# Performance work log

Hardware: AMD Instinct MI355X
Metric: run time of the kernel (lower is better)

## Reference

```python
import jax, jax.numpy as jnp
from jax import lax
import numpy as np

B, L, T = 128, 4096, 48


def setup_inputs() -> dict:
    key = jax.random.key(0)
    k1, k2 = jax.random.split(key)
    inputs = jax.random.normal(k1, (B, L, T), dtype=jnp.float32)
    # glorot_uniform init for [T, T] transition matrix
    limit = float(np.sqrt(6.0 / (T + T)))
    transition_params = jax.random.uniform(k2, (T, T), dtype=jnp.float32,
                                           minval=-limit, maxval=limit)
    return {"inputs": inputs, "transition_params": transition_params}


def crf_decode(potentials, transitions):
    # potentials: [B, Lp, T]; transitions: [T, T]
    first = potentials[:, 0, :]                       # [B, T]
    rest = jnp.swapaxes(potentials[:, 1:, :], 0, 1)   # [Lp-1, B, T]

    def fwd_step(state, emit):
        # state: [B, T] scores for previous tag; transitions[i, j]: i -> j
        scores = state[:, :, None] + transitions[None, :, :]  # [B, T, T]
        bp = jnp.argmax(scores, axis=1).astype(jnp.int32)     # [B, T]
        new_state = jnp.max(scores, axis=1) + emit            # [B, T]
        return new_state, bp

    last, bps = lax.scan(fwd_step, first, rest)  # bps: [Lp-1, B, T]
    last_tag = jnp.argmax(last, axis=-1).astype(jnp.int32)    # [B]
    best_score = jnp.max(last, axis=-1)                       # [B]

    def back_step(tag, bp):
        # tag: [B] tag at step t+1; bp: [B, T] backpointers into step t
        prev = jnp.take_along_axis(bp, tag[:, None], axis=1)[:, 0]
        return prev, prev

    _, tags_prefix = lax.scan(back_step, last_tag, bps, reverse=True)  # [Lp-1, B]
    tags = jnp.concatenate([tags_prefix, last_tag[None, :]], axis=0)   # [Lp, B]
    return jnp.swapaxes(tags, 0, 1), best_score


def reference(inputs, transition_params):
    pot = inputs[:, 1:-1, :]  # drop first/last positions, [B, L-2, T]
    tags_id, _ = crf_decode(pot, transition_params)
    return (pot, transition_params, tags_id)
```

## Files before the change

kernel.cpp:

```cpp
#include <hip/hip_runtime.h>
#include <stdint.h>

#define BATCH 128
#define LFULL 4096
#define TT 48
#define NPOT 4094
#define NBP  4093
#define SEG  64
#define NSEG 64
#define SLOT 192

__global__ __launch_bounds__(64, 1) void k_forward(const float* __restrict__ in,
                                                   const float* __restrict__ trans,
                                                   char* __restrict__ statesBase,
                                                   unsigned char* __restrict__ bound) {
    const int b = blockIdx.x;
    const int lane = threadIdx.x;
    const int kk = (lane < TT) ? lane : 0;

    __shared__ __align__(16) float lsw[2][64];

    float tcol[TT];
#pragma unroll
    for (int j = 0; j < TT; ++j) tcol[j] = trans[j * TT + kk];

#define PIN_TCOL() \
    asm volatile("" \
        : "+v"(tcol[0]),  "+v"(tcol[1]),  "+v"(tcol[2]),  "+v"(tcol[3]),  \
          "+v"(tcol[4]),  "+v"(tcol[5]),  "+v"(tcol[6]),  "+v"(tcol[7]),  \
          "+v"(tcol[8]),  "+v"(tcol[9]),  "+v"(tcol[10]), "+v"(tcol[11]), \
          "+v"(tcol[12]), "+v"(tcol[13]), "+v"(tcol[14]), "+v"(tcol[15]), \
          "+v"(tcol[16]), "+v"(tcol[17]), "+v"(tcol[18]), "+v"(tcol[19]), \
          "+v"(tcol[20]), "+v"(tcol[21]), "+v"(tcol[22]), "+v"(tcol[23]), \
          "+v"(tcol[24]), "+v"(tcol[25]), "+v"(tcol[26]), "+v"(tcol[27]), \
          "+v"(tcol[28]), "+v"(tcol[29]), "+v"(tcol[30]), "+v"(tcol[31]), \
          "+v"(tcol[32]), "+v"(tcol[33]), "+v"(tcol[34]), "+v"(tcol[35]), \
          "+v"(tcol[36]), "+v"(tcol[37]), "+v"(tcol[38]), "+v"(tcol[39]), \
          "+v"(tcol[40]), "+v"(tcol[41]), "+v"(tcol[42]), "+v"(tcol[43]), \
          "+v"(tcol[44]), "+v"(tcol[45]), "+v"(tcol[46]), "+v"(tcol[47]))

    const float* inb = in + (size_t)b * (LFULL * TT);
    char* sb = statesBase + (size_t)b * NBP * SLOT;

    float s0 = inb[TT + kk];
    lsw[0][lane] = s0;
    if (lane < TT) ((float*)sb)[lane] = s0;

    auto STEP = [&](int P, int t, float e, bool snap) {
        float c[TT];
#pragma unroll
        for (int j = 0; j < 12; ++j) {
            float4 v = *(const float4*)(&lsw[P][4 * j]);
            c[4*j+0] = v.x + tcol[4*j+0];
            c[4*j+1] = v.y + tcol[4*j+1];
            c[4*j+2] = v.z + tcol[4*j+2];
            c[4*j+3] = v.w + tcol[4*j+3];
        }
        float r[16];
#pragma unroll
        for (int g = 0; g < 16; ++g)
            r[g] = fmaxf(fmaxf(c[3*g], c[3*g+1]), c[3*g+2]);
        float u0 = fmaxf(fmaxf(r[0], r[1]), r[2]);
        float u1 = fmaxf(fmaxf(r[3], r[4]), r[5]);
        float u2 = fmaxf(fmaxf(r[6], r[7]), r[8]);
        float u3 = fmaxf(fmaxf(r[9], r[10]), r[11]);
        float u4 = fmaxf(fmaxf(r[12], r[13]), r[14]);
        float u5 = fmaxf(r[15], u0);
        float w0 = fmaxf(fmaxf(u1, u2), u3);
        float w1 = fmaxf(u4, u5);
        float snew = fmaxf(w0, w1) + e;
        lsw[P ^ 1][lane] = snew;
        if (snap && lane < TT)
            *(float*)(sb + (size_t)t * SLOT + (size_t)lane * 4) = snew;
    };

    auto LD = [&](int t) -> float {
        int tc = (t <= NBP) ? t : NBP;
        return inb[(size_t)(tc + 1) * TT + kk];
    };

    float e0 = LD(1), e1 = LD(2), e2 = LD(3), e3 = LD(4);
    float e4 = LD(5), e5 = LD(6), e6 = LD(7), e7 = LD(8);
    int t = 1;
    for (; t + 7 <= NBP; t += 8) {
        PIN_TCOL();
        STEP(0, t,     e0, true); e0 = LD(t + 8);
        STEP(1, t + 1, e1, true); e1 = LD(t + 9);
        STEP(0, t + 2, e2, true); e2 = LD(t + 10);
        STEP(1, t + 3, e3, true); e3 = LD(t + 11);
        STEP(0, t + 4, e4, true); e4 = LD(t + 12);
        STEP(1, t + 5, e5, true); e5 = LD(t + 13);
        STEP(0, t + 6, e6, true); e6 = LD(t + 14);
        STEP(1, t + 7, e7, true); e7 = LD(t + 15);
    }
    PIN_TCOL();
    STEP(0, 4089, e0, true);
    STEP(1, 4090, e1, true);
    STEP(0, 4091, e2, true);
    STEP(1, 4092, e3, true);
    STEP(0, 4093, e4, false);

    if (lane == 0) {
        float best = lsw[1][0]; int bi = 0;
#pragma unroll
        for (int j = 1; j < TT; ++j) {
            float v = lsw[1][j];
            if (v > best) { best = v; bi = j; }
        }
        bound[b * (NSEG + 1) + NSEG] = (unsigned char)bi;
    }
#undef PIN_TCOL
}

#define CHUNK 16
__global__ __launch_bounds__(256) void k_bp(const float* __restrict__ trans,
                                            char* __restrict__ statesBase) {
    const int lane = threadIdx.x & 63;
    const int wv = threadIdx.x >> 6;
    const int b = blockIdx.y * 4 + wv;
    const int i0 = blockIdx.x * CHUNK;
    const int kk = (lane < TT) ? lane : 0;

    __shared__ float ldsT[TT * TT];
    for (int i = threadIdx.x; i < TT * TT; i += 256) ldsT[i] = trans[i];
    __syncthreads();

    float tcol[TT];
#pragma unroll
    for (int j = 0; j < TT; ++j) tcol[j] = ldsT[j * TT + kk];

    char* sb = statesBase + (size_t)b * NBP * SLOT;

    for (int ii = 0; ii < CHUNK; ++ii) {
        int i = i0 + ii;
        if (i >= NBP) break;
        const float* sp = (const float*)(sb + (size_t)i * SLOT);
        float sv[TT];
#pragma unroll
        for (int j = 0; j < TT; j += 4) {
            float4 v = *(const float4*)(sp + j);
            sv[j] = v.x; sv[j+1] = v.y; sv[j+2] = v.z; sv[j+3] = v.w;
        }
        float best = sv[0] + tcol[0]; int bi = 0;
#pragma unroll
        for (int j = 1; j < TT; ++j) {
            float v = sv[j] + tcol[j];
            if (v > best) { best = v; bi = j; }
        }
        if (lane < TT)
            *(unsigned char*)(sb + (size_t)i * SLOT + lane) = (unsigned char)bi;
    }
}

__global__ __launch_bounds__(64) void k_compose(const char* __restrict__ statesBase,
                                                unsigned char* __restrict__ G) {
    const int s = blockIdx.x, b = blockIdx.y;
    const int i0 = s * SEG;
    const int cnt = (SEG < NBP - i0) ? SEG : (NBP - i0);
    const int lane = threadIdx.x;

    __shared__ unsigned char lbp[SEG * TT];
    const char* sb = statesBase + (size_t)b * NBP * SLOT;
    for (int ii = 0; ii < cnt; ++ii) {
        if (lane < 12)
            ((uint32_t*)lbp)[ii * 12 + lane] =
                *(const uint32_t*)(sb + (size_t)(i0 + ii) * SLOT + (size_t)lane * 4);
    }
    __syncthreads();

    if (lane < TT) {
        int M = lane;
        for (int ii = cnt - 1; ii >= 0; --ii) M = lbp[ii * TT + M];
        G[(b * NSEG + s) * TT + lane] = (unsigned char)M;
    }
}

__global__ void k_boundary(const unsigned char* __restrict__ G,
                           unsigned char* __restrict__ bound) {
    int b = threadIdx.x;
    int x = bound[b * (NSEG + 1) + NSEG];
    for (int s = NSEG - 1; s >= 0; --s) {
        x = G[(b * NSEG + s) * TT + x];
        bound[b * (NSEG + 1) + s] = x;
    }
}

__global__ __launch_bounds__(64) void k_fill(const char* __restrict__ statesBase,
                                             const unsigned char* __restrict__ bound,
                                             float* __restrict__ tags) {
    const int s = blockIdx.x, b = blockIdx.y;
    const int i0 = s * SEG;
    const int cnt = (SEG < NBP - i0) ? SEG : (NBP - i0);
    const int lane = threadIdx.x;

    __shared__ unsigned char lbp[SEG * TT];
    const char* sb = statesBase + (size_t)b * NBP * SLOT;
    for (int ii = 0; ii < cnt; ++ii) {
        if (lane < 12)
            ((uint32_t*)lbp)[ii * 12 + lane] =
                *(const uint32_t*)(sb + (size_t)(i0 + ii) * SLOT + (size_t)lane * 4);
    }
    __syncthreads();

    if (lane == 0) {
        int x = bound[b * (NSEG + 1) + s + 1];
        if (s == NSEG - 1)
            tags[(size_t)b * NPOT + (NPOT - 1)] = (float)x;
        for (int ii = cnt - 1; ii >= 0; --ii) {
            x = lbp[ii * TT + x];
            tags[(size_t)b * NPOT + i0 + ii] = (float)x;
        }
    }
}

__global__ __launch_bounds__(256) void k_copy(const float* __restrict__ in,
                                              const float* __restrict__ trans,
                                              float* __restrict__ out) {
    const int potN4 = (BATCH * NPOT * TT) / 4;
    const int rowN = NPOT * TT;
    int idx = blockIdx.x * 256 + threadIdx.x;
    if (idx < potN4) {
        int p4 = idx * 4;
        int b = p4 / rowN;
        int off = p4 - b * rowN;
        float4 v = *(const float4*)(in + (size_t)b * (LFULL * TT) + off + TT);
        *(float4*)(out + p4) = v;
    } else if (idx < potN4 + (TT * TT) / 4) {
        int q = idx - potN4;
        *(float4*)(out + (size_t)BATCH * NPOT * TT + (size_t)q * 4) =
            *(const float4*)(trans + (size_t)q * 4);
    }
}

extern "C" void kernel_launch(void* const* d_in, const int* in_sizes, int n_in,
                              void* d_out, int out_size, void* d_ws, size_t ws_size,
                              hipStream_t stream) {
    (void)in_sizes; (void)n_in; (void)d_ws; (void)ws_size; (void)out_size;

    const float* in = (const float*)d_in[0];
    const float* trans = (const float*)d_in[1];
    float* out = (float*)d_out;

    char* statesBase = (char*)d_out;
    unsigned char* bound = (unsigned char*)(out + (size_t)BATCH * NPOT * TT);
    unsigned char* G = (unsigned char*)(out + (size_t)BATCH * NPOT * TT + TT * TT);
    float* tags = out + (size_t)BATCH * NPOT * TT + TT * TT;

    k_forward <<<dim3(BATCH),        dim3(64),  0, stream>>>(in, trans, statesBase, bound);
    k_bp      <<<dim3(256, 32),      dim3(256), 0, stream>>>(trans, statesBase);
    k_compose <<<dim3(NSEG, BATCH),  dim3(64),  0, stream>>>(statesBase, G);
    k_boundary<<<dim3(1),            dim3(BATCH), 0, stream>>>(G, bound);
    k_fill    <<<dim3(NSEG, BATCH),  dim3(64),  0, stream>>>(statesBase, bound, tags);

    int total4 = (BATCH * NPOT * TT) / 4 + (TT * TT) / 4;
    k_copy    <<<dim3((total4 + 255) / 256), dim3(256), 0, stream>>>(in, trans, out);
}
```

Measured before the change: 1.425 ms.

## Interleave two batch rows per wave in forward Viterbi recurrence

Each forward wavefront now processes two batch elements in alternation, so the dependent max-plus chain of one row can overlap the LDS round-trip and latency of the other. The state vector is re-read from LDS into registers right after each write, and the max reduction is reshaped into groups of four. This halves the grid to 64 blocks and doubles register use for the state copies. On a GPU with many compute units that lowers occupancy and parallelism, in exchange for more latency hiding per wave.

New measurement: 1.895 ms. 1.33x slower.

```diff
diff --git a/kernel.cpp b/kernel.cpp
--- a/kernel.cpp
+++ b/kernel.cpp
@@ -14,9 +14,10 @@
                                                    const float* __restrict__ trans,
                                                    char* __restrict__ statesBase,
                                                    unsigned char* __restrict__ bound) {
-    const int b = blockIdx.x;
     const int lane = threadIdx.x;
     const int kk = (lane < TT) ? lane : 0;
+    const int bA = blockIdx.x * 2;
+    const int bB = bA + 1;
 
     __shared__ __align__(16) float lsw[2][64];
 
@@ -39,75 +40,101 @@
           "+v"(tcol[40]), "+v"(tcol[41]), "+v"(tcol[42]), "+v"(tcol[43]), \
           "+v"(tcol[44]), "+v"(tcol[45]), "+v"(tcol[46]), "+v"(tcol[47]))
 
-    const float* inb = in + (size_t)b * (LFULL * TT);
-    char* sb = statesBase + (size_t)b * NBP * SLOT;
-
-    float s0 = inb[TT + kk];
-    lsw[0][lane] = s0;
-    if (lane < TT) ((float*)sb)[lane] = s0;
-
-    auto STEP = [&](int P, int t, float e, bool snap) {
-        float c[TT];
+    PIN_TCOL();
+
+    const float* inA = in + (size_t)bA * (LFULL * TT);
+    const float* inB = in + (size_t)bB * (LFULL * TT);
+    char* sA = statesBase + (size_t)bA * NBP * SLOT;
+    char* sB = statesBase + (size_t)bB * NBP * SLOT;
+
+    float4 rdA[12], rdB[12];
+#pragma unroll
+    for (int j = 0; j < 12; ++j) {
+        rdA[j] = *(const float4*)(inA + TT + 4 * j);
+        rdB[j] = *(const float4*)(inB + TT + 4 * j);
+    }
+    if (lane < TT) {
+        ((float*)sA)[lane] = inA[TT + lane];
+        ((float*)sB)[lane] = inB[TT + lane];
+    }
+
+    auto STEP = [&](int c, float4* rd, char* sb, int t, float e) {
+        float g0, g1, g2, g3, g4, g5, g6, g7, g8, g9, g10, g11;
+        {
+            float a, b2, c2, d;
+#define GRP(i, dst) \
+            a  = rd[i].x + tcol[4*i+0]; \
+            b2 = rd[i].y + tcol[4*i+1]; \
+            c2 = rd[i].z + tcol[4*i+2]; \
+            d  = rd[i].w + tcol[4*i+3]; \
+            dst = fmaxf(fmaxf(a, b2), fmaxf(c2, d));
+            GRP(0, g0)  GRP(1, g1)  GRP(2, g2)  GRP(3, g3)
+            GRP(4, g4)  GRP(5, g5)  GRP(6, g6)  GRP(7, g7)
+            GRP(8, g8)  GRP(9, g9)  GRP(10, g10) GRP(11, g11)
+#undef GRP
+        }
+        float n0 = fmaxf(fmaxf(g0, g1), g2);
+        float n1 = fmaxf(fmaxf(g3, g4), g5);
+        float n2 = fmaxf(fmaxf(g6, g7), g8);
+        float n3 = fmaxf(fmaxf(g9, g10), g11);
+        float snew = fmaxf(fmaxf(n0, n1), fmaxf(n2, n3)) + e;
+
+        lsw[c][lane] = snew;
+        if (t <= NBP - 1 && lane < TT)
+            *(float*)(sb + (size_t)t * SLOT + (size_t)lane * 4) = snew;
+#pragma unroll
+        for (int j = 0; j < 12; ++j)
+            rd[j] = *(const float4*)(&lsw[c][4 * j]);
+    };
+
+    auto LDA = [&](int t) -> float {
+        int tc = (t <= NBP) ? t : NBP;
+        return inA[(size_t)(tc + 1) * TT + kk];
+    };
+    auto LDB = [&](int t) -> float {
+        int tc = (t <= NBP) ? t : NBP;
+        return inB[(size_t)(tc + 1) * TT + kk];
+    };
+
+    float eA0 = LDA(1), eA1 = LDA(2), eA2 = LDA(3), eA3 = LDA(4);
+    float eB0 = LDB(1), eB1 = LDB(2), eB2 = LDB(3), eB3 = LDB(4);
+
+    int t = 1;
+    for (; t + 3 <= NBP; t += 4) {
+        STEP(0, rdA, sA, t,     eA0); eA0 = LDA(t + 4);
+        STEP(1, rdB, sB, t,     eB0); eB0 = LDB(t + 4);
+        STEP(0, rdA, sA, t + 1, eA1); eA1 = LDA(t + 5);
+        STEP(1, rdB, sB, t + 1, eB1); eB1 = LDB(t + 5);
+        STEP(0, rdA, sA, t + 2, eA2); eA2 = LDA(t + 6);
+        STEP(1, rdB, sB, t + 2, eB2); eB2 = LDB(t + 6);
+        STEP(0, rdA, sA, t + 3, eA3); eA3 = LDA(t + 7);
+        STEP(1, rdB, sB, t + 3, eB3); eB3 = LDB(t + 7);
+        PIN_TCOL();
+    }
+    STEP(0, rdA, sA, NBP, eA0);
+    STEP(1, rdB, sB, NBP, eB0);
+
+    if (lane == 0) {
+        float best = rdA[0].x; int bi = 0;
 #pragma unroll
         for (int j = 0; j < 12; ++j) {
-            float4 v = *(const float4*)(&lsw[P][4 * j]);
-            c[4*j+0] = v.x + tcol[4*j+0];
-            c[4*j+1] = v.y + tcol[4*j+1];
-            c[4*j+2] = v.z + tcol[4*j+2];
-            c[4*j+3] = v.w + tcol[4*j+3];
-        }
-        float r[16];
-#pragma unroll
-        for (int g = 0; g < 16; ++g)
-            r[g] = fmaxf(fmaxf(c[3*g], c[3*g+1]), c[3*g+2]);
-        float u0 = fmaxf(fmaxf(r[0], r[1]), r[2]);
-        float u1 = fmaxf(fmaxf(r[3], r[4]), r[5]);
-        float u2 = fmaxf(fmaxf(r[6], r[7]), r[8]);
-        float u3 = fmaxf(fmaxf(r[9], r[10]), r[11]);
-        float u4 = fmaxf(fmaxf(r[12], r[13]), r[14]);
-        float u5 = fmaxf(r[15], u0);
-        float w0 = fmaxf(fmaxf(u1, u2), u3);
-        float w1 = fmaxf(u4, u5);
-        float snew = fmaxf(w0, w1) + e;
-        lsw[P ^ 1][lane] = snew;
-        if (snap && lane < TT)
-            *(float*)(sb + (size_t)t * SLOT + (size_t)lane * 4) = snew;
-    };
-
-    auto LD = [&](int t) -> float {
-        int tc = (t <= NBP) ? t : NBP;
-        return inb[(size_t)(tc + 1) * TT + kk];
-    };
-
-    float e0 = LD(1), e1 = LD(2), e2 = LD(3), e3 = LD(4);
-    float e4 = LD(5), e5 = LD(6), e6 = LD(7), e7 = LD(8);
-    int t = 1;
-    for (; t + 7 <= NBP; t += 8) {
-        PIN_TCOL();
-        STEP(0, t,     e0, true); e0 = LD(t + 8);
-        STEP(1, t + 1, e1, true); e1 = LD(t + 9);
-        STEP(0, t + 2, e2, true); e2 = LD(t + 10);
-        STEP(1, t + 3, e3, true); e3 = LD(t + 11);
-        STEP(0, t + 4, e4, true); e4 = LD(t + 12);
-        STEP(1, t + 5, e5, true); e5 = LD(t + 13);
-        STEP(0, t + 6, e6, true); e6 = LD(t + 14);
-        STEP(1, t + 7, e7, true); e7 = LD(t + 15);
-    }
-    PIN_TCOL();
-    STEP(0, 4089, e0, true);
-    STEP(1, 4090, e1, true);
-    STEP(0, 4091, e2, true);
-    STEP(1, 4092, e3, true);
-    STEP(0, 4093, e4, false);
-
-    if (lane == 0) {
-        float best = lsw[1][0]; int bi = 0;
-#pragma unroll
-        for (int j = 1; j < TT; ++j) {
-            float v = lsw[1][j];
-            if (v > best) { best = v; bi = j; }
-        }
-        bound[b * (NSEG + 1) + NSEG] = (unsigned char)bi;
+            float v;
+            v = rdA[j].x; if (4*j+0 > 0 && v > best) { best = v; bi = 4*j+0; }
+            v = rdA[j].y; if (v > best) { best = v; bi = 4*j+1; }
+            v = rdA[j].z; if (v > best) { best = v; bi = 4*j+2; }
+            v = rdA[j].w; if (v > best) { best = v; bi = 4*j+3; }
+        }
+        bound[bA * (NSEG + 1) + NSEG] = (unsigned char)bi;
+        best = rdB[0].x; bi = 0;
+#pragma unroll
+        for (int j = 0; j < 12; ++j) {
+            float v;
+            v = rdB[j].x; if (4*j+0 > 0 && v > best) { best = v; bi = 4*j+0; }
+            v = rdB[j].y; if (v > best) { best = v; bi = 4*j+1; }
+            v = rdB[j].z; if (v > best) { best = v; bi = 4*j+2; }
+            v = rdB[j].w; if (v > best) { best = v; bi = 4*j+3; }
+        }
+        bound[bB * (NSEG + 1) + NSEG] = (unsigned char)bi;
     }
 #undef PIN_TCOL
 }
@@ -246,7 +273,7 @@
     unsigned char* G = (unsigned char*)(out + (size_t)BATCH * NPOT * TT + TT * TT);
     float* tags = out + (size_t)BATCH * NPOT * TT + TT * TT;
 
-    k_forward <<<dim3(BATCH),        dim3(64),  0, stream>>>(in, trans, statesBase, bound);
+    k_forward <<<dim3(BATCH / 2),    dim3(64),  0, stream>>>(in, trans, statesBase, bound);
     k_bp      <<<dim3(256, 32),      dim3(256), 0, stream>>>(trans, statesBase);
     k_compose <<<dim3(NSEG, BATCH),  dim3(64),  0, stream>>>(statesBase, G);
     k_boundary<<<dim3(1),            dim3(BATCH), 0, stream>>>(G, bound);
```
